# Kernel tuning notes

Hardware: AMD Instinct MI355X
Metric: run time of the kernel (lower is better)

Reference implementation:

```python
import jax, jax.numpy as jnp
import numpy as np
import math

B, S, D, H = 1, 4096, 1024, 16
DH = D // H  # head_dim = 64
NEG = -10000.0  # matches torch masked-fill value in source (not -inf)


def setup_inputs() -> dict:
    key = jax.random.key(0)
    ks = jax.random.split(key, 5)
    scale = 0.02
    return {
        "x": jax.random.normal(ks[0], (B, S, D), dtype=jnp.float32),
        "Wqkv_w": jax.random.normal(ks[1], (3 * D, D), dtype=jnp.float32) * scale,
        "Wqkv_b": jax.random.normal(ks[2], (3 * D,), dtype=jnp.float32) * scale,
        "out_w": jax.random.normal(ks[3], (D, D), dtype=jnp.float32) * scale,
        "out_b": jax.random.normal(ks[4], (D,), dtype=jnp.float32) * scale,
    }


def reference(x, Wqkv_w, Wqkv_b, out_w, out_b):
    # QKV projection: (B,S,D) @ (D,3D) + b -> (B,S,3,H,DH)
    qkv = jnp.einsum('bsd,ed->bse', x, Wqkv_w) + Wqkv_b
    qkv = qkv.reshape(B, S, 3, H, DH)
    q, k, v = qkv[:, :, 0], qkv[:, :, 1], qkv[:, :, 2]  # each (B,S,H,DH)
    softmax_scale = 1.0 / math.sqrt(DH)
    # scores: (B,H,T,S)
    scores = jnp.einsum('bthd,bshd->bhts', q, k * softmax_scale)
    # causal additive mask with -10000 above diagonal (faithful to source)
    causal_mask = jnp.triu(jnp.full((S, S), NEG, dtype=scores.dtype), k=1)
    scores = scores + causal_mask
    attention = jax.nn.softmax(scores, axis=-1)
    context = jnp.einsum('bhts,bshd->bthd', attention, v)  # (B,T,H,DH)
    context = context.reshape(B, S, D)
    out = jnp.einsum('bsd,ed->bse', context, out_w) + out_b
    return out
```

## Files before the change

kernel.cpp:

```cpp
#include <hip/hip_runtime.h>
#include <hip/hip_bf16.h>

using f32x4  = __attribute__((ext_vector_type(4))) float;
using f32x16 = __attribute__((ext_vector_type(16))) float;
using bf16x8 = __attribute__((ext_vector_type(8))) __bf16;
using u16x8  = __attribute__((ext_vector_type(8))) unsigned short;
using u32x4  = __attribute__((ext_vector_type(4))) unsigned int;

#define DEV __device__ __forceinline__

constexpr int S_  = 4096;
constexpr int D_  = 1024;
constexpr int KD  = 1024;

constexpr size_t XB_OFF   = 0;
constexpr size_t WQKV_OFF = 8388608;
constexpr size_t WOUT_OFF = 14680064;
constexpr size_t QB_OFF   = 16777216;
constexpr size_t KB_OFF   = 25165824;
constexpr size_t VT_OFF   = 33554432;
constexpr size_t CTX_OFF  = 41943040;

DEV unsigned short f2bf(float f) {
  __hip_bfloat16 h = __float2bfloat16(f);
  return __builtin_bit_cast(unsigned short, h);
}

DEV void gl_lds16(const void* g, void* l) {
  __builtin_amdgcn_global_load_lds(
      (const __attribute__((address_space(1))) void*)g,
      (__attribute__((address_space(3))) void*)l, 16, 0, 0);
}

DEV f32x4 mfma16(bf16x8 a, bf16x8 b, f32x4 c) {
  return __builtin_amdgcn_mfma_f32_16x16x32_bf16(a, b, c, 0, 0, 0);
}
DEV f32x16 mfma32(bf16x8 a, bf16x8 b, f32x16 c) {
  return __builtin_amdgcn_mfma_f32_32x32x16_bf16(a, b, c, 0, 0, 0);
}
DEV unsigned cvtpk(float lo, float hi) {
  unsigned r;
  asm("v_cvt_pk_bf16_f32 %0, %1, %2" : "=v"(r) : "v"(lo), "v"(hi));
  return r;
}
DEV float exp2_fast(float x) {
  float r;
  asm("v_exp_f32 %0, %1" : "=v"(r) : "v"(x));
  return r;
}
DEV void pl32(unsigned& a, unsigned& b) {
  asm("v_permlane32_swap_b32 %0, %1" : "+v"(a), "+v"(b));
}
DEV float xhalf_add(float x) {
  float y;
  asm("v_mov_b32 %0, %1" : "=v"(y) : "v"(x));
  unsigned a = __builtin_bit_cast(unsigned, x), b = __builtin_bit_cast(unsigned, y);
  pl32(a, b);
  return __builtin_bit_cast(float, a) + __builtin_bit_cast(float, b);
}

__global__ void cvt_all_k(const float* __restrict__ x,
                          const float* __restrict__ wq,
                          const float* __restrict__ wo,
                          unsigned short* __restrict__ xb,
                          unsigned short* __restrict__ wqb,
                          unsigned short* __restrict__ wob) {
  for (int u = blockIdx.x * 256 + threadIdx.x; u < 1048576; u += 2048 * 256) {
    const float* s; unsigned short* d; int off;
    if (u < 524288)      { s = x;  d = xb;  off = u; }
    else if (u < 917504) { s = wq; d = wqb; off = u - 524288; }
    else                 { s = wo; d = wob; off = u - 917504; }
    const float4* s4 = (const float4*)s;
    float4 a = s4[2 * off], b = s4[2 * off + 1];
    u16x8 o;
    o[0] = f2bf(a.x); o[1] = f2bf(a.y); o[2] = f2bf(a.z); o[3] = f2bf(a.w);
    o[4] = f2bf(b.x); o[5] = f2bf(b.y); o[6] = f2bf(b.z); o[7] = f2bf(b.w);
    ((u16x8*)d)[off] = o;
  }
}

__global__ __launch_bounds__(512)
void gemm_qkv_k(const unsigned short* __restrict__ A,
                const unsigned short* __restrict__ Bt,
                const float* __restrict__ bias,
                unsigned short* __restrict__ qb,
                unsigned short* __restrict__ kb,
                unsigned short* __restrict__ vt) {
  __shared__ unsigned short As[2][4096];
  __shared__ unsigned short Bs[2][4096];
  const int t = threadIdx.x;
  const int w = t >> 6, l = t & 63;
  const int lr = l & 15, lg = l >> 4, lk = lg * 8;
  const int m0 = blockIdx.y * 128, n0 = blockIdx.x * 128;
  const int wm = (w >> 2) * 64, wn = (w & 3) * 32;

  f32x4 acc[4][2] = {};

  const int srow = t >> 2;
  const int scolb = (t & 3) << 4;
  const char* Ag = (const char*)A + (size_t)(m0 + srow) * (KD * 2) + scolb;
  const char* Bg = (const char*)Bt + (size_t)(n0 + srow) * (KD * 2) + scolb;

  auto stage = [&](int buf, int kt) {
    gl_lds16(Ag + kt * 64, (char*)&As[buf][0] + t * 16);
    gl_lds16(Bg + kt * 64, (char*)&Bs[buf][0] + t * 16);
  };

  stage(0, 0);
  for (int kt = 0; kt < KD / 32; ++kt) {
    __syncthreads();
    if (kt + 1 < KD / 32) stage((kt + 1) & 1, kt + 1);
    const int buf = kt & 1;

    bf16x8 a[4], bb[2];
#pragma unroll
    for (int mi = 0; mi < 4; ++mi)
      a[mi] = *(const bf16x8*)&As[buf][(wm + mi * 16 + lr) * 32 + lk];
#pragma unroll
    for (int ni = 0; ni < 2; ++ni)
      bb[ni] = *(const bf16x8*)&Bs[buf][(wn + ni * 16 + lr) * 32 + lk];
#pragma unroll
    for (int mi = 0; mi < 4; ++mi)
#pragma unroll
      for (int ni = 0; ni < 2; ++ni)
        acc[mi][ni] = mfma16(a[mi], bb[ni], acc[mi][ni]);
  }

  const int r0 = lg * 4;
  const int which = n0 >> 10;
  const float kscale = 0.125f * 1.44269504088896f;
#pragma unroll
  for (int mi = 0; mi < 4; ++mi) {
    const int sbase = m0 + wm + mi * 16 + r0;
#pragma unroll
    for (int ni = 0; ni < 2; ++ni) {
      const int e = n0 + wn + ni * 16 + lr;
      const float bv = bias[e];
      const int h = (e & 1023) >> 6, dd = e & 63;
#pragma unroll
      for (int r = 0; r < 4; ++r) {
        const float v = acc[mi][ni][r] + bv;
        const int sr = sbase + r;
        if (which == 0)      qb[((size_t)(h * S_ + sr)) * 64 + dd] = f2bf(v);
        else if (which == 1) kb[((size_t)(h * S_ + sr)) * 64 + dd] = f2bf(v * kscale);
        else                 vt[((size_t)(h * 64 + dd)) * S_ + sr] = f2bf(v);
      }
    }
  }
}

__global__ __launch_bounds__(512)
void gemm_proj_k(const unsigned short* __restrict__ A,
                 const unsigned short* __restrict__ Bt,
                 const float* __restrict__ bias,
                 float* __restrict__ outf) {
  __shared__ unsigned short As[2][4096];
  __shared__ unsigned short Bs[2][2048];
  const int t = threadIdx.x;
  const int w = t >> 6, l = t & 63;
  const int lr = l & 15, lg = l >> 4, lk = lg * 8;
  const int m0 = blockIdx.y * 128, n0 = blockIdx.x * 64;
  const int wm = (w >> 1) * 32, wn = (w & 1) * 32;

  f32x4 acc[2][2] = {};

  const int srow = t >> 2;
  const int scolb = (t & 3) << 4;
  const char* Ag = (const char*)A + (size_t)(m0 + srow) * (KD * 2) + scolb;
  const char* Bg = (const char*)Bt + (size_t)(n0 + (srow & 63)) * (KD * 2) + scolb;

  auto stage = [&](int buf, int kt) {
    gl_lds16(Ag + kt * 64, (char*)&As[buf][0] + t * 16);
    if (t < 256) gl_lds16(Bg + kt * 64, (char*)&Bs[buf][0] + t * 16);
  };

  stage(0, 0);
  for (int kt = 0; kt < KD / 32; ++kt) {
    __syncthreads();
    if (kt + 1 < KD / 32) stage((kt + 1) & 1, kt + 1);
    const int buf = kt & 1;

    bf16x8 a[2], bb[2];
#pragma unroll
    for (int mi = 0; mi < 2; ++mi)
      a[mi] = *(const bf16x8*)&As[buf][(wm + mi * 16 + lr) * 32 + lk];
#pragma unroll
    for (int ni = 0; ni < 2; ++ni)
      bb[ni] = *(const bf16x8*)&Bs[buf][(wn + ni * 16 + lr) * 32 + lk];
#pragma unroll
    for (int mi = 0; mi < 2; ++mi)
#pragma unroll
      for (int ni = 0; ni < 2; ++ni)
        acc[mi][ni] = mfma16(a[mi], bb[ni], acc[mi][ni]);
  }

  const int r0 = lg * 4;
#pragma unroll
  for (int mi = 0; mi < 2; ++mi) {
    const int sbase = m0 + wm + mi * 16 + r0;
#pragma unroll
    for (int ni = 0; ni < 2; ++ni) {
      const int e = n0 + wn + ni * 16 + lr;
      const float bv = bias[e];
#pragma unroll
      for (int r = 0; r < 4; ++r)
        outf[(size_t)(sbase + r) * D_ + e] = acc[mi][ni][r] + bv;
    }
  }
}

__global__ __launch_bounds__(512, 4)
void attn_k(const unsigned short* __restrict__ Qb,
            const unsigned short* __restrict__ Kb,
            const unsigned short* __restrict__ Vt,
            unsigned short* __restrict__ ctx) {
  __shared__ char smem[65536];

  const int t = threadIdx.x;
  const int w8 = t >> 6;
  const int g  = w8 >> 2;
  const int w  = w8 & 3;
  const int l = t & 63, lq = l & 31, hi = l >> 5;
  const int b = blockIdx.x + (blockIdx.y << 5);
  const int h = ((b & 7) << 1) | ((b >> 3) & 1);
  const int qi = b >> 4;
  const int bi = qi < 16 ? (31 - qi) : (qi - 16);

  const int sg = t >> 8;
  const int ts = t & 255;
  const int srow = ts >> 3;
  const int ssw  = ((ts & 7) << 4) ^ ((srow & 7) << 4);
  const char* Kg0 = (const char*)Kb + (size_t)(h * S_) * 128;
  const char* Vg0 = (const char*)Vt + (size_t)(h * 64) * (size_t)(S_ * 2);

  const int q0 = bi * 128;
  const int qrow = q0 + w * 32 + lq;
  const int qwmin = q0 + w * 32, qwmax = qwmin + 31;
  const int niter = bi + 1;

  const unsigned short* Qr = Qb + ((size_t)(h * S_ + qrow)) * 64;
  bf16x8 qf[4];
#pragma unroll
  for (int d0 = 0; d0 < 4; ++d0)
    qf[d0] = *(const bf16x8*)(Qr + d0 * 16 + hi * 8);

  f32x16 cacc[2] = {};
  float lsum = 0.f;

  auto stage = [&](int buf, int tl) {
    const int kv0 = tl * 64;
    char* kd = smem + sg * 16384 + buf * 8192;
    const char* Kg = Kg0 + (size_t)kv0 * 128;
    gl_lds16(Kg + (size_t)srow * 128 + ssw,        kd + ts * 16);
    gl_lds16(Kg + (size_t)(32 + srow) * 128 + ssw, kd + 4096 + ts * 16);
    char* vd = smem + 32768 + sg * 16384 + buf * 8192;
    const char* Vg = Vg0 + (size_t)kv0 * 2;
    gl_lds16(Vg + (size_t)srow * (S_ * 2) + ssw,        vd + ts * 16);
    gl_lds16(Vg + (size_t)(32 + srow) * (S_ * 2) + ssw, vd + 4096 + ts * 16);
  };

  int cur = 0;
  stage(0, sg * niter);

  for (int it = 0; it < niter; ++it) {
    __syncthreads();
    if (it + 1 < niter) stage(cur ^ 1, it + 1 + sg * niter);
    const char* Kt = smem + g * 16384 + cur * 8192;
    const char* Vl = smem + 32768 + g * 16384 + cur * 8192;
    const int tl = it + g * niter;

    if (tl * 64 + 63 <= qwmin) {
      f32x16 st0, st1;
#pragma unroll
      for (int r = 0; r < 16; ++r) { st0[r] = -8.0f; st1[r] = -8.0f; }
      const char* kb0 = Kt + lq * 128;
      const char* kb1 = Kt + (32 + lq) * 128;
      const int ksw = (lq & 7) << 4;
      __builtin_amdgcn_s_setprio(1);
#pragma unroll
      for (int d0 = 0; d0 < 4; ++d0) {
        bf16x8 kf0 = *(const bf16x8*)(kb0 + ((d0 * 32 + hi * 16) ^ ksw));
        bf16x8 kf1 = *(const bf16x8*)(kb1 + ((d0 * 32 + hi * 16) ^ ksw));
        st0 = mfma32(kf0, qf[d0], st0);
        st1 = mfma32(kf1, qf[d0], st1);
      }
      __builtin_amdgcn_s_setprio(0);

#pragma unroll
      for (int r = 0; r < 16; ++r) { st0[r] = exp2_fast(st0[r]); st1[r] = exp2_fast(st1[r]); }
      float a0 = (st0[0] + st0[1]) + (st0[2] + st0[3]);
      float a1 = (st0[4] + st0[5]) + (st0[6] + st0[7]);
      float a2 = (st0[8] + st0[9]) + (st0[10] + st0[11]);
      float a3 = (st0[12] + st0[13]) + (st0[14] + st0[15]);
      float b0 = (st1[0] + st1[1]) + (st1[2] + st1[3]);
      float b1 = (st1[4] + st1[5]) + (st1[6] + st1[7]);
      float b2 = (st1[8] + st1[9]) + (st1[10] + st1[11]);
      float b3 = (st1[12] + st1[13]) + (st1[14] + st1[15]);
      lsum += xhalf_add(((a0 + a1) + (a2 + a3)) + ((b0 + b1) + (b2 + b3)));

      unsigned x0 = cvtpk(st0[0], st0[1]),   x1 = cvtpk(st0[2], st0[3]);
      unsigned y0 = cvtpk(st0[4], st0[5]),   y1 = cvtpk(st0[6], st0[7]);
      pl32(x0, y0); pl32(x1, y1);
      u32x4 f00 = {x0, x1, y0, y1};
      bf16x8 pf00 = __builtin_bit_cast(bf16x8, f00);
      unsigned x2 = cvtpk(st0[8], st0[9]),   x3 = cvtpk(st0[10], st0[11]);
      unsigned y2 = cvtpk(st0[12], st0[13]), y3 = cvtpk(st0[14], st0[15]);
      pl32(x2, y2); pl32(x3, y3);
      u32x4 f01 = {x2, x3, y2, y3};
      bf16x8 pf01 = __builtin_bit_cast(bf16x8, f01);
      unsigned u0 = cvtpk(st1[0], st1[1]),    u1 = cvtpk(st1[2], st1[3]);
      unsigned v0w = cvtpk(st1[4], st1[5]),   v1w = cvtpk(st1[6], st1[7]);
      pl32(u0, v0w); pl32(u1, v1w);
      u32x4 f10 = {u0, u1, v0w, v1w};
      bf16x8 pf10 = __builtin_bit_cast(bf16x8, f10);
      unsigned u2 = cvtpk(st1[8], st1[9]),    u3 = cvtpk(st1[10], st1[11]);
      unsigned v2w = cvtpk(st1[12], st1[13]), v3w = cvtpk(st1[14], st1[15]);
      pl32(u2, v2w); pl32(u3, v3w);
      u32x4 f11 = {u2, u3, v2w, v3w};
      bf16x8 pf11 = __builtin_bit_cast(bf16x8, f11);

      __builtin_amdgcn_s_setprio(1);
#pragma unroll
      for (int db = 0; db < 2; ++db) {
        const int dr = db * 32 + lq;
        const char* vbase = Vl + dr * 128;
        const int vsw = (dr & 7) << 4;
        bf16x8 va = *(const bf16x8*)(vbase + ((hi * 16) ^ vsw));
        bf16x8 vb = *(const bf16x8*)(vbase + ((32 + hi * 16) ^ vsw));
        bf16x8 vc = *(const bf16x8*)(vbase + ((64 + hi * 16) ^ vsw));
        bf16x8 vd = *(const bf16x8*)(vbase + ((96 + hi * 16) ^ vsw));
        cacc[db] = mfma32(va, pf00, cacc[db]);
        cacc[db] = mfma32(vb, pf01, cacc[db]);
        cacc[db] = mfma32(vc, pf10, cacc[db]);
        cacc[db] = mfma32(vd, pf11, cacc[db]);
      }
      __builtin_amdgcn_s_setprio(0);
    } else {
#pragma unroll
      for (int kvh = 0; kvh < 2; ++kvh) {
        const int kv0s = tl * 64 + kvh * 32;
        if (kv0s > qwmax) continue;

        f32x16 st;
#pragma unroll
        for (int r = 0; r < 16; ++r) st[r] = -8.0f;
        const int kr = kvh * 32 + lq;
        const char* kbase = Kt + kr * 128;
        const int ksw = (kr & 7) << 4;
#pragma unroll
        for (int d0 = 0; d0 < 4; ++d0) {
          bf16x8 kf = *(const bf16x8*)(kbase + ((d0 * 32 + hi * 16) ^ ksw));
          st = mfma32(kf, qf[d0], st);
        }

        if (kv0s + 31 > qwmin) {
#pragma unroll
          for (int r = 0; r < 16; ++r) {
            const int kvg = kv0s + (r & 3) + 8 * (r >> 2) + 4 * hi;
            if (kvg > qrow) st[r] = -INFINITY;
          }
        }

#pragma unroll
        for (int r = 0; r < 16; ++r) st[r] = exp2_fast(st[r]);
        float a0 = (st[0] + st[1]) + (st[2] + st[3]);
        float a1 = (st[4] + st[5]) + (st[6] + st[7]);
        float a2 = (st[8] + st[9]) + (st[10] + st[11]);
        float a3 = (st[12] + st[13]) + (st[14] + st[15]);
        lsum += xhalf_add((a0 + a1) + (a2 + a3));

        unsigned x0 = cvtpk(st[0], st[1]),   x1 = cvtpk(st[2], st[3]);
        unsigned y0 = cvtpk(st[4], st[5]),   y1 = cvtpk(st[6], st[7]);
        pl32(x0, y0); pl32(x1, y1);
        u32x4 f0 = {x0, x1, y0, y1};
        bf16x8 pf0 = __builtin_bit_cast(bf16x8, f0);
        unsigned x2 = cvtpk(st[8], st[9]),   x3 = cvtpk(st[10], st[11]);
        unsigned y2 = cvtpk(st[12], st[13]), y3 = cvtpk(st[14], st[15]);
        pl32(x2, y2); pl32(x3, y3);
        u32x4 f1 = {x2, x3, y2, y3};
        bf16x8 pf1 = __builtin_bit_cast(bf16x8, f1);

#pragma unroll
        for (int db = 0; db < 2; ++db) {
          const int dr = db * 32 + lq;
          const char* vbase = Vl + dr * 128;
          const int vsw = (dr & 7) << 4;
          bf16x8 v0 = *(const bf16x8*)(vbase + ((kvh * 64 + hi * 16) ^ vsw));
          bf16x8 v1 = *(const bf16x8*)(vbase + ((kvh * 64 + 32 + hi * 16) ^ vsw));
          cacc[db] = mfma32(v0, pf0, cacc[db]);
          cacc[db] = mfma32(v1, pf1, cacc[db]);
        }
      }
    }
    cur ^= 1;
  }

  __syncthreads();
  float* slot = (float*)smem + (size_t)(w * 64 + l) * 36;
  if (g == 1) {
    slot[0] = lsum;
#pragma unroll
    for (int j = 0; j < 16; ++j) { slot[1 + j] = cacc[0][j]; slot[17 + j] = cacc[1][j]; }
  }
  __syncthreads();
  if (g == 0) {
    const float inv = 1.0f / (lsum + slot[0]);
    unsigned short* base = ctx + (size_t)qrow * D_ + h * 64;
#pragma unroll
    for (int db = 0; db < 2; ++db)
#pragma unroll
      for (int r = 0; r < 16; r += 2) {
        const float o0 = (cacc[db][r]     + slot[1 + db * 16 + r])     * inv;
        const float o1 = (cacc[db][r + 1] + slot[1 + db * 16 + r + 1]) * inv;
        const unsigned wv = cvtpk(o0, o1);
        const int d = (r & 3) + 8 * (r >> 2) + 4 * hi + 32 * db;
        *(unsigned*)(base + d) = wv;
      }
  }
}

extern "C" void kernel_launch(void* const* d_in, const int* in_sizes, int n_in,
                              void* d_out, int out_size, void* d_ws, size_t ws_size,
                              hipStream_t stream) {
  const float* x      = (const float*)d_in[0];
  const float* Wqkv_w = (const float*)d_in[1];
  const float* Wqkv_b = (const float*)d_in[2];
  const float* out_w  = (const float*)d_in[3];
  const float* out_b  = (const float*)d_in[4];
  float* out = (float*)d_out;
  char* ws = (char*)d_ws;

  unsigned short* xb    = (unsigned short*)(ws + XB_OFF);
  unsigned short* wqkvb = (unsigned short*)(ws + WQKV_OFF);
  unsigned short* woutb = (unsigned short*)(ws + WOUT_OFF);
  unsigned short* Qb    = (unsigned short*)(ws + QB_OFF);
  unsigned short* Kb    = (unsigned short*)(ws + KB_OFF);
  unsigned short* Vt    = (unsigned short*)(ws + VT_OFF);
  unsigned short* ctx   = (unsigned short*)(ws + CTX_OFF);

  cvt_all_k<<<2048, 256, 0, stream>>>(x, Wqkv_w, out_w, xb, wqkvb, woutb);

  gemm_qkv_k<<<dim3(24, 32), 512, 0, stream>>>(xb, wqkvb, Wqkv_b, Qb, Kb, Vt);

  attn_k<<<dim3(32, 16), 512, 0, stream>>>(Qb, Kb, Vt, ctx);

  gemm_proj_k<<<dim3(16, 32), 512, 0, stream>>>(ctx, woutb, out_b, out);
}
```

Measured before the change: 120.5 us.

## Enlarge QKV GEMM tile to 256x256 with 4-stage LDS pipeline

Result: slower. 134.7 us (+11.7%).

```diff
diff --git a/kernel.cpp b/kernel.cpp
--- a/kernel.cpp
+++ b/kernel.cpp
@@ -79,50 +79,64 @@
   }
 }
 
-__global__ __launch_bounds__(512)
+__global__ __launch_bounds__(512, 2)
 void gemm_qkv_k(const unsigned short* __restrict__ A,
                 const unsigned short* __restrict__ Bt,
                 const float* __restrict__ bias,
                 unsigned short* __restrict__ qb,
                 unsigned short* __restrict__ kb,
                 unsigned short* __restrict__ vt) {
-  __shared__ unsigned short As[2][4096];
-  __shared__ unsigned short Bs[2][4096];
+  __shared__ char smem[131072];
   const int t = threadIdx.x;
   const int w = t >> 6, l = t & 63;
-  const int lr = l & 15, lg = l >> 4, lk = lg * 8;
-  const int m0 = blockIdx.y * 128, n0 = blockIdx.x * 128;
-  const int wm = (w >> 2) * 64, wn = (w & 3) * 32;
-
-  f32x4 acc[4][2] = {};
+  const int lr = l & 15, lg = l >> 4;
+  const int m0 = blockIdx.y * 256, n0 = blockIdx.x * 256;
+  const int wm = (w >> 2) * 128, wn = (w & 3) * 64;
+
+  f32x4 acc[8][4] = {};
 
   const int srow = t >> 2;
   const int scolb = (t & 3) << 4;
   const char* Ag = (const char*)A + (size_t)(m0 + srow) * (KD * 2) + scolb;
   const char* Bg = (const char*)Bt + (size_t)(n0 + srow) * (KD * 2) + scolb;
-
-  auto stage = [&](int buf, int kt) {
-    gl_lds16(Ag + kt * 64, (char*)&As[buf][0] + t * 16);
-    gl_lds16(Bg + kt * 64, (char*)&Bs[buf][0] + t * 16);
+  const size_t rstep = (size_t)128 * (KD * 2);
+
+  auto stage = [&](int kt) {
+    char* base = smem + (kt & 3) * 32768;
+    const char* as = Ag + kt * 64;
+    gl_lds16(as,         base + t * 16);
+    gl_lds16(as + rstep, base + 8192 + t * 16);
+    const char* bs = Bg + kt * 64;
+    gl_lds16(bs,         base + 16384 + t * 16);
+    gl_lds16(bs + rstep, base + 24576 + t * 16);
   };
 
-  stage(0, 0);
+  stage(0);
+  stage(1);
+
   for (int kt = 0; kt < KD / 32; ++kt) {
-    __syncthreads();
-    if (kt + 1 < KD / 32) stage((kt + 1) & 1, kt + 1);
-    const int buf = kt & 1;
-
-    bf16x8 a[4], bb[2];
-#pragma unroll
-    for (int mi = 0; mi < 4; ++mi)
-      a[mi] = *(const bf16x8*)&As[buf][(wm + mi * 16 + lr) * 32 + lk];
-#pragma unroll
-    for (int ni = 0; ni < 2; ++ni)
-      bb[ni] = *(const bf16x8*)&Bs[buf][(wn + ni * 16 + lr) * 32 + lk];
-#pragma unroll
-    for (int mi = 0; mi < 4; ++mi)
-#pragma unroll
-      for (int ni = 0; ni < 2; ++ni)
+    if (kt + 2 < KD / 32) {
+      stage(kt + 2);
+      asm volatile("s_waitcnt vmcnt(8)" ::: "memory");
+    } else if (kt + 1 < KD / 32) {
+      asm volatile("s_waitcnt vmcnt(4)" ::: "memory");
+    } else {
+      asm volatile("s_waitcnt vmcnt(0)" ::: "memory");
+    }
+    __builtin_amdgcn_s_barrier();
+
+    const char* base = smem + (kt & 3) * 32768;
+    bf16x8 a[8], bb[4];
+#pragma unroll
+    for (int mi = 0; mi < 8; ++mi)
+      a[mi] = *(const bf16x8*)(base + (wm + mi * 16 + lr) * 64 + lg * 16);
+#pragma unroll
+    for (int ni = 0; ni < 4; ++ni)
+      bb[ni] = *(const bf16x8*)(base + 16384 + (wn + ni * 16 + lr) * 64 + lg * 16);
+#pragma unroll
+    for (int mi = 0; mi < 8; ++mi)
+#pragma unroll
+      for (int ni = 0; ni < 4; ++ni)
         acc[mi][ni] = mfma16(a[mi], bb[ni], acc[mi][ni]);
   }
 
@@ -130,10 +144,10 @@
   const int which = n0 >> 10;
   const float kscale = 0.125f * 1.44269504088896f;
 #pragma unroll
-  for (int mi = 0; mi < 4; ++mi) {
+  for (int mi = 0; mi < 8; ++mi) {
     const int sbase = m0 + wm + mi * 16 + r0;
 #pragma unroll
-    for (int ni = 0; ni < 2; ++ni) {
+    for (int ni = 0; ni < 4; ++ni) {
       const int e = n0 + wn + ni * 16 + lr;
       const float bv = bias[e];
       const int h = (e & 1023) >> 6, dd = e & 63;
@@ -440,7 +454,7 @@
 
   cvt_all_k<<<2048, 256, 0, stream>>>(x, Wqkv_w, out_w, xb, wqkvb, woutb);
 
-  gemm_qkv_k<<<dim3(24, 32), 512, 0, stream>>>(xb, wqkvb, Wqkv_b, Qb, Kb, Vt);
+  gemm_qkv_k<<<dim3(12, 16), 512, 0, stream>>>(xb, wqkvb, Wqkv_b, Qb, Kb, Vt);
 
   attn_k<<<dim3(32, 16), 512, 0, stream>>>(Qb, Kb, Vt, ctx);
 
```
